# Kernel optimization log

Measured on AMD Instinct MI355X. Metric: run time of the kernel, lower is better.

The kernel has to match this reference:

```python
import jax, jax.numpy as jnp
import numpy as np

B, S, D = 4, 2048, 128


def setup_inputs() -> dict:
    key = jax.random.key(0)
    kq, kk, kv = jax.random.split(key, 3)
    query = jax.random.normal(kq, (B, S, D), dtype=jnp.float32)
    key_t = jax.random.normal(kk, (B, S, D), dtype=jnp.float32)
    value = jax.random.normal(kv, (B, S, D), dtype=jnp.float32)
    return {"query": query, "key": key_t, "value": value}


def reference(query, key, value):
    # Raw dot-general attention: contract only the last dim, NO batch dims,
    # so scores have shape [B, Sq, B, Sk] (cross-batch attention).
    scores = jnp.einsum('aqd,bkd->aqbk', query, key)  # [B,S,B,S]
    # softmax over the trailing half of the dims (axes 2 and 3 jointly)
    attn = jax.nn.softmax(scores, axis=(2, 3))
    # Dropout: train=False -> deterministic no-op.
    # Second dot_general contracts trailing (B,Sk) of attn with leading (B,Sk) of value.
    y = jnp.einsum('aqbk,bkd->aqd', attn, value)  # [B,S,D]
    return y
```

## Files before the change

kernel.cpp:

```cpp
#include <hip/hip_runtime.h>
#include <hip/hip_bf16.h>

#define NROWS 8192
#define DH    128
#define G     8
#define KPG   1024
#define NIT   (KPG / 32)
#define LOG2E 1.44269504088896340736f
#define MSCALED (56.0f * LOG2E)

typedef __attribute__((ext_vector_type(8))) short    short8;
typedef __attribute__((ext_vector_type(4))) float    floatx4;
typedef __attribute__((ext_vector_type(4))) unsigned short us4;
typedef __attribute__((ext_vector_type(8))) _Float16 half8;
typedef __attribute__((ext_vector_type(4))) _Float16 half4;

#define MFMA_BF(a, b, c)  __builtin_amdgcn_mfma_f32_16x16x32_bf16((a), (b), (c), 0, 0, 0)
#define MFMA_F16(a, b, c) __builtin_amdgcn_mfma_f32_16x16x32_f16((a), (b), (c), 0, 0, 0)

__device__ __forceinline__ unsigned short f32_to_bf16(float f) {
    union { float f; unsigned u; } v; v.f = f;
    unsigned u = v.u + 0x7FFFu + ((v.u >> 16) & 1u);
    return (unsigned short)(u >> 16);
}
__device__ __forceinline__ float bf16_to_f32(unsigned short h) {
    union { unsigned u; float f; } v; v.u = ((unsigned)h) << 16;
    return v.f;
}
__device__ __forceinline__ void async_ld16(const void* g, void* lds) {
    __builtin_amdgcn_global_load_lds(
        (const __attribute__((address_space(1))) unsigned int*)g,
        (__attribute__((address_space(3))) unsigned int*)lds, 16, 0, 0);
}

__global__ void prep_kernel(const float* __restrict__ Q, const float* __restrict__ K,
                            const float* __restrict__ V,
                            _Float16* __restrict__ Qh, _Float16* __restrict__ Ql,
                            _Float16* __restrict__ Kf, unsigned short* __restrict__ VT) {
    int bid = blockIdx.x;
    if (bid < 1024) {
        int i = bid * 1024 + threadIdx.x * 4;
        float4 q = *(const float4*)(Q + i);
        float4 k = *(const float4*)(K + i);
        half4 qh, ql, kf;
        float qv[4] = {q.x, q.y, q.z, q.w};
        float kv[4] = {k.x, k.y, k.z, k.w};
#pragma unroll
        for (int j = 0; j < 4; j++) {
            _Float16 h = (_Float16)qv[j];
            qh[j] = h;
            ql[j] = (_Float16)(qv[j] - (float)h);
            kf[j] = (_Float16)kv[j];
        }
        *(half4*)(Qh + i) = qh;
        *(half4*)(Ql + i) = ql;
        *(half4*)(Kf + i) = kf;
        return;
    }
    int b2 = bid - 1024;
    int by = b2 >> 7, bx = b2 & 127;
    if (by == 2) {
        int t = bx * 256 + threadIdx.x;
        int base = t * 4;
        int row = base >> 13;
        unsigned short v = (row == 0) ? (unsigned short)0x3F80 : (unsigned short)0;
        us4 val = {v, v, v, v};
        *(us4*)(VT + (size_t)(128 + row) * NROWS + (base & 8191)) = val;
        return;
    }
    __shared__ unsigned short tile[64][68];
    const int r0 = bx * 64;
    const int d0 = by * 64;
    const int t = threadIdx.x;
    const int col4 = (t & 15) * 4;
    const int rstart = t >> 4;
#pragma unroll
    for (int rr = rstart; rr < 64; rr += 16) {
        float4 v = *(const float4*)(V + (size_t)(r0 + rr) * DH + d0 + col4);
        tile[rr][col4 + 0] = f32_to_bf16(v.x);
        tile[rr][col4 + 1] = f32_to_bf16(v.y);
        tile[rr][col4 + 2] = f32_to_bf16(v.z);
        tile[rr][col4 + 3] = f32_to_bf16(v.w);
    }
    __syncthreads();
    const int d = t >> 2;
    const int rc = (t & 3) * 16;
    unsigned short* dst = VT + (size_t)(d0 + d) * NROWS + r0 + rc;
    short8 a, b;
#pragma unroll
    for (int j = 0; j < 8; j++) a[j] = tile[rc + j][d];
#pragma unroll
    for (int j = 0; j < 8; j++) b[j] = tile[rc + 8 + j][d];
    *(short8*)dst = a;
    *((short8*)dst + 1) = b;
}

__launch_bounds__(256, 2)
__global__ void attn_kernel(const _Float16* __restrict__ Qh, const _Float16* __restrict__ Ql,
                            const _Float16* __restrict__ Kf,
                            const unsigned short* __restrict__ VT,
                            unsigned short* __restrict__ Opart,
                            float* __restrict__ lsum) {
    __shared__ __align__(16) unsigned short kvbuf[2][17 * 512];
    __shared__ __align__(16) unsigned short pbuf[4][32][40];

    const int lane = threadIdx.x & 63;
    const int wave = threadIdx.x >> 6;
    const int g    = blockIdx.x & 7;
    const int qt   = blockIdx.x >> 3;
    const int l15 = lane & 15, l4 = lane >> 4;
    const int kb = g * KPG;
    const int qrow0 = qt * 128 + wave * 32;

    half8 qh[2][4], ql[2][4];
#pragma unroll
    for (int rs = 0; rs < 2; rs++) {
        const half8* ph = (const half8*)(Qh + (size_t)(qrow0 + rs * 16 + l15) * DH + l4 * 8);
        const half8* pl = (const half8*)(Ql + (size_t)(qrow0 + rs * 16 + l15) * DH + l4 * 8);
#pragma unroll
        for (int c = 0; c < 4; c++) { qh[rs][c] = ph[c * 4]; ql[rs][c] = pl[c * 4]; }
    }

    floatx4 Oacc[2][9];
#pragma unroll
    for (int rs = 0; rs < 2; rs++)
#pragma unroll
        for (int n = 0; n < 9; n++) Oacc[rs][n] = (floatx4){0.f, 0.f, 0.f, 0.f};

    auto stage = [&](int k0, int buf) {
        unsigned short* dst = kvbuf[buf];
        for (int s = wave; s < 17; s += 4) {
            const void* gp;
            if (s < 8)
                gp = Kf + (size_t)(k0 + (s >> 2) * 16 + l15) * DH + (s & 3) * 32 + l4 * 8;
            else
                gp = VT + (size_t)((s - 8) * 16 + l15) * NROWS + k0 + l4 * 8;
            async_ld16(gp, dst + s * 512);
        }
    };

    stage(kb, 0);
    for (int it = 0; it < NIT; ++it) {
        __syncthreads();
        if (it + 1 < NIT) stage(kb + (it + 1) * 32, (it + 1) & 1);

        const unsigned short* cb = kvbuf[it & 1];

        floatx4 S[2][2];
        S[0][0] = S[0][1] = S[1][0] = S[1][1] = (floatx4){0.f, 0.f, 0.f, 0.f};
#pragma unroll
        for (int c = 0; c < 4; c++) {
            half8 b0 = *(const half8*)(cb + c * 512 + lane * 8);
            half8 b1 = *(const half8*)(cb + (4 + c) * 512 + lane * 8);
            S[0][0] = MFMA_F16(qh[0][c], b0, S[0][0]);
            S[0][0] = MFMA_F16(ql[0][c], b0, S[0][0]);
            S[1][0] = MFMA_F16(qh[1][c], b0, S[1][0]);
            S[1][0] = MFMA_F16(ql[1][c], b0, S[1][0]);
            S[0][1] = MFMA_F16(qh[0][c], b1, S[0][1]);
            S[0][1] = MFMA_F16(ql[0][c], b1, S[0][1]);
            S[1][1] = MFMA_F16(qh[1][c], b1, S[1][1]);
            S[1][1] = MFMA_F16(ql[1][c], b1, S[1][1]);
        }

#pragma unroll
        for (int rs = 0; rs < 2; rs++)
#pragma unroll
            for (int r = 0; r < 4; r++) {
                float p0 = exp2f(__builtin_fmaf(S[rs][0][r], LOG2E, -MSCALED));
                float p1 = exp2f(__builtin_fmaf(S[rs][1][r], LOG2E, -MSCALED));
                pbuf[wave][rs * 16 + l4 * 4 + r][l15]      = f32_to_bf16(p0);
                pbuf[wave][rs * 16 + l4 * 4 + r][16 + l15] = f32_to_bf16(p1);
            }
        short8 pf0 = *(const short8*)(&pbuf[wave][l15][l4 * 8]);
        short8 pf1 = *(const short8*)(&pbuf[wave][16 + l15][l4 * 8]);

#pragma unroll
        for (int n = 0; n < 9; n++) {
            short8 vf = *(const short8*)(cb + (8 + n) * 512 + lane * 8);
            Oacc[0][n] = MFMA_BF(pf0, vf, Oacc[0][n]);
            Oacc[1][n] = MFMA_BF(pf1, vf, Oacc[1][n]);
        }
    }

    unsigned short* op = Opart + ((size_t)g * NROWS + qrow0) * DH;
#pragma unroll
    for (int rs = 0; rs < 2; rs++)
#pragma unroll
        for (int n = 0; n < 8; n++)
#pragma unroll
            for (int r = 0; r < 4; r++)
                op[(rs * 16 + l4 * 4 + r) * DH + n * 16 + l15] = f32_to_bf16(Oacc[rs][n][r]);
    if (l15 == 0) {
#pragma unroll
        for (int rs = 0; rs < 2; rs++)
#pragma unroll
            for (int r = 0; r < 4; r++)
                lsum[(size_t)g * NROWS + qrow0 + rs * 16 + l4 * 4 + r] = Oacc[rs][8][r];
    }
}

__global__ void merge_kernel(const unsigned short* __restrict__ Opart,
                             const float* __restrict__ lsum, float* __restrict__ out) {
    int t = blockIdx.x * 256 + threadIdx.x;
    int base = t * 8;
    int q = base >> 7;
    float L = 0.f;
#pragma unroll
    for (int g = 0; g < G; g++) L += lsum[(size_t)g * NROWS + q];
    float acc[8] = {0.f, 0.f, 0.f, 0.f, 0.f, 0.f, 0.f, 0.f};
#pragma unroll
    for (int g = 0; g < G; g++) {
        short8 v = *(const short8*)(Opart + (size_t)g * NROWS * DH + base);
#pragma unroll
        for (int j = 0; j < 8; j++) acc[j] += bf16_to_f32((unsigned short)v[j]);
    }
    float inv = 1.0f / L;
    float4 o0 = {acc[0] * inv, acc[1] * inv, acc[2] * inv, acc[3] * inv};
    float4 o1 = {acc[4] * inv, acc[5] * inv, acc[6] * inv, acc[7] * inv};
    *(float4*)(out + base) = o0;
    *(float4*)(out + base + 4) = o1;
}

extern "C" void kernel_launch(void* const* d_in, const int* in_sizes, int n_in,
                              void* d_out, int out_size, void* d_ws, size_t ws_size,
                              hipStream_t stream) {
    const float* Q = (const float*)d_in[0];
    const float* K = (const float*)d_in[1];
    const float* V = (const float*)d_in[2];
    float* out = (float*)d_out;

    char* ws = (char*)d_ws;
    const size_t SZH = (size_t)NROWS * DH * sizeof(_Float16);
    _Float16* Qh = (_Float16*)(ws);
    _Float16* Ql = (_Float16*)(ws + SZH);
    _Float16* Kf = (_Float16*)(ws + 2 * SZH);
    unsigned short* VT = (unsigned short*)(ws + 3 * SZH);
    char* p = ws + 3 * SZH + (size_t)144 * NROWS * sizeof(unsigned short);
    unsigned short* Opart = (unsigned short*)p;
    float* lsum = (float*)(p + (size_t)G * NROWS * DH * sizeof(unsigned short));

    hipLaunchKernelGGL(prep_kernel, dim3(1024 + 384), dim3(256), 0, stream,
                       Q, K, V, Qh, Ql, Kf, VT);
    hipLaunchKernelGGL(attn_kernel, dim3((NROWS / 128) * G), dim3(256), 0, stream,
                       Qh, Ql, Kf, VT, Opart, lsum);
    hipLaunchKernelGGL(merge_kernel, dim3(NROWS * DH / (256 * 8)), dim3(256), 0, stream,
                       Opart, lsum, out);
}
```

Baseline: 139.4 us.

## Process 64 keys per iteration with interleaved V layout and packed bf16 P writes

Doubles the key block per pipeline stage from 32 to 64, halving the number of barriers and stage calls and doubling LDS buffer size. The V transpose in prep now interleaves key pairs so each lane's P values for adjacent key columns can be packed into one 32-bit bf16x2 store, and exp2f is replaced with raw v_exp_f32. This cuts sync and LDS-store overhead per key. In exchange it raises LDS use, which may hurt occupancy at two blocks per CU, and the fast exp drops denormal handling.

```diff
diff --git a/kernel.cpp b/kernel.cpp
--- a/kernel.cpp
+++ b/kernel.cpp
@@ -1,11 +1,12 @@
 #include <hip/hip_runtime.h>
 #include <hip/hip_bf16.h>
+#include <string.h>
 
 #define NROWS 8192
 #define DH    128
 #define G     8
 #define KPG   1024
-#define NIT   (KPG / 32)
+#define NIT   (KPG / 64)
 #define LOG2E 1.44269504088896340736f
 #define MSCALED (56.0f * LOG2E)
 
@@ -26,6 +27,9 @@
 __device__ __forceinline__ float bf16_to_f32(unsigned short h) {
     union { unsigned u; float f; } v; v.u = ((unsigned)h) << 16;
     return v.f;
+}
+__device__ __forceinline__ float fast_exp2(float x) {
+    float r; asm("v_exp_f32 %0, %1" : "=v"(r) : "v"(x)); return r;
 }
 __device__ __forceinline__ void async_ld16(const void* g, void* lds) {
     __builtin_amdgcn_global_load_lds(
@@ -85,12 +89,20 @@
     __syncthreads();
     const int d = t >> 2;
     const int rc = (t & 3) * 16;
+    const int sb = rc >> 5;
+    const int q0 = rc & 31;
     unsigned short* dst = VT + (size_t)(d0 + d) * NROWS + r0 + rc;
     short8 a, b;
 #pragma unroll
-    for (int j = 0; j < 8; j++) a[j] = tile[rc + j][d];
-#pragma unroll
-    for (int j = 0; j < 8; j++) b[j] = tile[rc + 8 + j][d];
+    for (int j = 0; j < 8; j++) {
+        int q = q0 + j;
+        a[j] = tile[sb * 32 + (q >> 1) + 16 * (q & 1)][d];
+    }
+#pragma unroll
+    for (int j = 0; j < 8; j++) {
+        int q = q0 + 8 + j;
+        b[j] = tile[sb * 32 + (q >> 1) + 16 * (q & 1)][d];
+    }
     *(short8*)dst = a;
     *((short8*)dst + 1) = b;
 }
@@ -101,7 +113,7 @@
                             const unsigned short* __restrict__ VT,
                             unsigned short* __restrict__ Opart,
                             float* __restrict__ lsum) {
-    __shared__ __align__(16) unsigned short kvbuf[2][17 * 512];
+    __shared__ __align__(16) unsigned short kvbuf[2][34 * 512];
     __shared__ __align__(16) unsigned short pbuf[4][32][40];
 
     const int lane = threadIdx.x & 63;
@@ -112,13 +124,13 @@
     const int kb = g * KPG;
     const int qrow0 = qt * 128 + wave * 32;
 
-    half8 qh[2][4], ql[2][4];
+    half8 qfh[2][4], qfl[2][4];
 #pragma unroll
     for (int rs = 0; rs < 2; rs++) {
         const half8* ph = (const half8*)(Qh + (size_t)(qrow0 + rs * 16 + l15) * DH + l4 * 8);
         const half8* pl = (const half8*)(Ql + (size_t)(qrow0 + rs * 16 + l15) * DH + l4 * 8);
 #pragma unroll
-        for (int c = 0; c < 4; c++) { qh[rs][c] = ph[c * 4]; ql[rs][c] = pl[c * 4]; }
+        for (int c = 0; c < 4; c++) { qfh[rs][c] = ph[c * 4]; qfl[rs][c] = pl[c * 4]; }
     }
 
     floatx4 Oacc[2][9];
@@ -129,12 +141,14 @@
 
     auto stage = [&](int k0, int buf) {
         unsigned short* dst = kvbuf[buf];
-        for (int s = wave; s < 17; s += 4) {
+        for (int s = wave; s < 34; s += 4) {
             const void* gp;
-            if (s < 8)
+            if (s < 16)
                 gp = Kf + (size_t)(k0 + (s >> 2) * 16 + l15) * DH + (s & 3) * 32 + l4 * 8;
-            else
-                gp = VT + (size_t)((s - 8) * 16 + l15) * NROWS + k0 + l4 * 8;
+            else {
+                int n = (s - 16) >> 1, h = (s - 16) & 1;
+                gp = VT + (size_t)(n * 16 + l15) * NROWS + k0 + h * 32 + l4 * 8;
+            }
             async_ld16(gp, dst + s * 512);
         }
     };
@@ -142,43 +156,47 @@
     stage(kb, 0);
     for (int it = 0; it < NIT; ++it) {
         __syncthreads();
-        if (it + 1 < NIT) stage(kb + (it + 1) * 32, (it + 1) & 1);
+        if (it + 1 < NIT) stage(kb + (it + 1) * 64, (it + 1) & 1);
 
         const unsigned short* cb = kvbuf[it & 1];
 
-        floatx4 S[2][2];
-        S[0][0] = S[0][1] = S[1][0] = S[1][1] = (floatx4){0.f, 0.f, 0.f, 0.f};
+        floatx4 S[2][4];
+#pragma unroll
+        for (int rs = 0; rs < 2; rs++)
+#pragma unroll
+            for (int kc = 0; kc < 4; kc++) S[rs][kc] = (floatx4){0.f, 0.f, 0.f, 0.f};
 #pragma unroll
         for (int c = 0; c < 4; c++) {
-            half8 b0 = *(const half8*)(cb + c * 512 + lane * 8);
-            half8 b1 = *(const half8*)(cb + (4 + c) * 512 + lane * 8);
-            S[0][0] = MFMA_F16(qh[0][c], b0, S[0][0]);
-            S[0][0] = MFMA_F16(ql[0][c], b0, S[0][0]);
-            S[1][0] = MFMA_F16(qh[1][c], b0, S[1][0]);
-            S[1][0] = MFMA_F16(ql[1][c], b0, S[1][0]);
-            S[0][1] = MFMA_F16(qh[0][c], b1, S[0][1]);
-            S[0][1] = MFMA_F16(ql[0][c], b1, S[0][1]);
-            S[1][1] = MFMA_F16(qh[1][c], b1, S[1][1]);
-            S[1][1] = MFMA_F16(ql[1][c], b1, S[1][1]);
-        }
-
-#pragma unroll
-        for (int rs = 0; rs < 2; rs++)
-#pragma unroll
-            for (int r = 0; r < 4; r++) {
-                float p0 = exp2f(__builtin_fmaf(S[rs][0][r], LOG2E, -MSCALED));
-                float p1 = exp2f(__builtin_fmaf(S[rs][1][r], LOG2E, -MSCALED));
-                pbuf[wave][rs * 16 + l4 * 4 + r][l15]      = f32_to_bf16(p0);
-                pbuf[wave][rs * 16 + l4 * 4 + r][16 + l15] = f32_to_bf16(p1);
+#pragma unroll
+            for (int kc = 0; kc < 4; kc++) {
+                half8 bk = *(const half8*)(cb + (kc * 4 + c) * 512 + lane * 8);
+                S[0][kc] = MFMA_F16(qfh[0][c], bk, S[0][kc]);
+                S[0][kc] = MFMA_F16(qfl[0][c], bk, S[0][kc]);
+                S[1][kc] = MFMA_F16(qfh[1][c], bk, S[1][kc]);
+                S[1][kc] = MFMA_F16(qfl[1][c], bk, S[1][kc]);
             }
-        short8 pf0 = *(const short8*)(&pbuf[wave][l15][l4 * 8]);
-        short8 pf1 = *(const short8*)(&pbuf[wave][16 + l15][l4 * 8]);
-
-#pragma unroll
-        for (int n = 0; n < 9; n++) {
-            short8 vf = *(const short8*)(cb + (8 + n) * 512 + lane * 8);
-            Oacc[0][n] = MFMA_BF(pf0, vf, Oacc[0][n]);
-            Oacc[1][n] = MFMA_BF(pf1, vf, Oacc[1][n]);
+        }
+
+#pragma unroll
+        for (int h = 0; h < 2; h++) {
+#pragma unroll
+            for (int rs = 0; rs < 2; rs++)
+#pragma unroll
+                for (int r = 0; r < 4; r++) {
+                    float pa = fast_exp2(__builtin_fmaf(S[rs][2 * h][r], LOG2E, -MSCALED));
+                    float pb = fast_exp2(__builtin_fmaf(S[rs][2 * h + 1][r], LOG2E, -MSCALED));
+                    __hip_bfloat162 pk = __float22bfloat162_rn(float2{pa, pb});
+                    unsigned u; memcpy(&u, &pk, 4);
+                    *(unsigned*)(&pbuf[wave][rs * 16 + l4 * 4 + r][2 * l15]) = u;
+                }
+            short8 pf0 = *(const short8*)(&pbuf[wave][l15][l4 * 8]);
+            short8 pf1 = *(const short8*)(&pbuf[wave][16 + l15][l4 * 8]);
+#pragma unroll
+            for (int n = 0; n < 9; n++) {
+                short8 vf = *(const short8*)(cb + (16 + n * 2 + h) * 512 + lane * 8);
+                Oacc[0][n] = MFMA_BF(pf0, vf, Oacc[0][n]);
+                Oacc[1][n] = MFMA_BF(pf1, vf, Oacc[1][n]);
+            }
         }
     }
 
```

After: 130.4 us. -6.4%, faster.
